# Performance work log

Measured on AMD Instinct MI355X. Metric: run time of the kernel, lower is better.

## Reference

```python
import jax, jax.numpy as jnp
import numpy as np
import math

B, T, C, H = 4, 2048, 1024, 16

def setup_inputs() -> dict:
    key = jax.random.key(0)
    ks = jax.random.split(key, 7)
    s = 0.02
    return {
        'x':  jax.random.normal(ks[0], (B, T, C), dtype=jnp.float32),
        'Wq': jax.random.normal(ks[1], (C, C), dtype=jnp.float32) * s,
        'bq': jnp.zeros((C,), dtype=jnp.float32),
        'Wk': jax.random.normal(ks[2], (C, C), dtype=jnp.float32) * s,
        'bk': jnp.zeros((C,), dtype=jnp.float32),
        'Wv': jax.random.normal(ks[3], (C, C), dtype=jnp.float32) * s,
        'bv': jnp.zeros((C,), dtype=jnp.float32),
    }

def reference(x, Wq, bq, Wk, bk, Wv, bv):
    # Dropouts are identity (eval mode). Note: the original module reuses
    # v_proj as the output projection -- reproduced faithfully.
    b, t, c = x.shape
    hs = c // H
    q = (x @ Wq + bq).reshape(b, t, H, hs).transpose(0, 2, 1, 3)  # [B,H,T,hs]
    k = (x @ Wk + bk).reshape(b, t, H, hs).transpose(0, 2, 1, 3)
    v = (x @ Wv + bv).reshape(b, t, H, hs).transpose(0, 2, 1, 3)
    att = jnp.einsum('bhqd,bhkd->bhqk', q, k) * (1.0 / math.sqrt(hs))
    causal = jnp.tril(jnp.ones((t, t), dtype=bool))
    att = jnp.where(causal[None, None], att, -jnp.inf)
    att = jax.nn.softmax(att, axis=-1)
    y = jnp.einsum('bhqk,bhkd->bhqd', att, v)  # [B,H,T,hs]
    y = y.transpose(0, 2, 1, 3).reshape(b, t, c)
    y = y @ Wv + bv  # module applies v_proj again as output projection
    return y
```

## Files before the change

kernel.cpp:

```cpp
#include <hip/hip_runtime.h>
#include <hip/hip_bf16.h>

typedef __bf16 bf16;
typedef __attribute__((ext_vector_type(8))) __bf16 bf16x8;
typedef __attribute__((ext_vector_type(4))) __bf16 bf16x4;
typedef __attribute__((ext_vector_type(2))) __bf16 bf16x2;
typedef __attribute__((ext_vector_type(4))) float f32x4;
typedef __attribute__((ext_vector_type(2))) unsigned int u32x2;
typedef __attribute__((ext_vector_type(4))) unsigned int u32x4;

#define MFMA16(a, b, c) __builtin_amdgcn_mfma_f32_16x16x32_bf16((a), (b), (c), 0, 0, 0)
#define SM_SCALE 0.18033688011112043f

__device__ __forceinline__ void gld_lds16(const bf16* g, bf16* l) {
    __builtin_amdgcn_global_load_lds((const __attribute__((address_space(1))) void*)g,
                                     (__attribute__((address_space(3))) void*)l, 16, 0, 0);
}

#define PBAR() asm volatile("s_barrier" ::: "memory")
#define VWAIT0() asm volatile("s_waitcnt vmcnt(0)" ::: "memory")

__global__ __launch_bounds__(256) void cvt_x(const float* __restrict__ in,
                                             bf16* __restrict__ outb, int n) {
    int i = (blockIdx.x * 256 + threadIdx.x) * 4;
    if (i + 3 < n) {
        const float4 v = *(const float4*)(in + i);
        bf16x4 o = {(bf16)v.x, (bf16)v.y, (bf16)v.z, (bf16)v.w};
        *(bf16x4*)(outb + i) = o;
    }
}

__global__ __launch_bounds__(256) void transpose_w3(const float* __restrict__ W0,
                                                    const float* __restrict__ W1,
                                                    const float* __restrict__ W2,
                                                    bf16* __restrict__ Wt) {
    const float* W = (blockIdx.z == 0) ? W0 : ((blockIdx.z == 1) ? W1 : W2);
    bf16* dst = Wt + (size_t)blockIdx.z * 1024 * 1024;
    __shared__ float tile[64][65];
    const int r0 = blockIdx.y * 64;
    const int c0 = blockIdx.x * 64;
    const int tid = threadIdx.x;
    for (int i = tid; i < 4096; i += 256) {
        int r = i >> 6, cc = i & 63;
        tile[r][cc] = W[(size_t)(r0 + r) * 1024 + c0 + cc];
    }
    __syncthreads();
    for (int i = tid; i < 4096; i += 256) {
        int n = i >> 6, k = i & 63;
        dst[(size_t)(c0 + n) * 1024 + r0 + k] = (bf16)tile[k][n];
    }
}

__global__ __launch_bounds__(512, 4) void gemm_qkv(const bf16* __restrict__ A,
                                                   const bf16* __restrict__ Bt,
                                                   const float* __restrict__ b0,
                                                   const float* __restrict__ b1,
                                                   const float* __restrict__ b2,
                                                   bf16* __restrict__ qb,
                                                   bf16* __restrict__ kb,
                                                   bf16* __restrict__ Vt) {
    __shared__ alignas(16) bf16 LDS[2 * 12288];

    const int orig = blockIdx.x;
    const int swz = (orig & 7) * 96 + (orig >> 3);
    const int by = swz / 24, bx = swz % 24;
    const int m0 = by * 256, n0 = bx * 128;

    const int tid = threadIdx.x;
    const int wid = tid >> 6, lane = tid & 63;
    const int wr = wid >> 1, wc = wid & 1;
    const int quad = lane >> 4, l16 = lane & 15;

    const int sr = tid >> 2;
    const int scol = (((tid & 3) ^ (sr & 3)) * 8);
    const bf16* gA = A + (size_t)(m0 + sr) * 1024 + scol;
    const bf16* gB = Bt + (size_t)(n0 + sr) * 1024 + scol;
    bf16* lA = &LDS[tid * 8];
    bf16* lB = &LDS[8192 + tid * 8];

    const int coff = ((quad ^ (l16 & 3)) * 8);

    f32x4 acc[4][4] = {};

    auto STAGE = [&](int kt, int p) {
        const int base = p * 12288;
        gld_lds16(gA + kt * 32, lA + base);
        gld_lds16(gA + kt * 32 + (size_t)128 * 1024, lA + base + 4096);
        gld_lds16(gB + kt * 32, lB + base);
    };

    STAGE(0, 0);
    VWAIT0();
    PBAR();

#pragma unroll 1
    for (int kt = 0; kt < 32; kt++) {
        const int p = kt & 1;
        const bf16* Asp = &LDS[p * 12288];
        const bf16* Bsp = Asp + 8192;
        if (kt + 1 < 32) STAGE(kt + 1, p ^ 1);

        bf16x8 af[4], bfr[4];
#pragma unroll
        for (int m4 = 0; m4 < 4; m4++)
            af[m4] = *(const bf16x8*)&Asp[(wr * 64 + m4 * 16 + l16) * 32 + coff];
#pragma unroll
        for (int ni = 0; ni < 4; ni++)
            bfr[ni] = *(const bf16x8*)&Bsp[(wc * 64 + ni * 16 + l16) * 32 + coff];

        __builtin_amdgcn_s_setprio(1);
#pragma unroll
        for (int m4 = 0; m4 < 4; m4++)
#pragma unroll
            for (int ni = 0; ni < 4; ni++)
                acc[m4][ni] = MFMA16(af[m4], bfr[ni], acc[m4][ni]);
        __builtin_amdgcn_s_setprio(0);

        if (kt + 1 < 32) VWAIT0();
        PBAR();
    }

    const int sel = n0 >> 10;
    const int nl0 = (n0 & 1023) + wc * 64;
    const int mb0 = m0 + wr * 64;
    if (sel < 2) {
        const float* bias = (sel == 0) ? b0 : b1;
        bf16* Cp = (sel == 0) ? qb : kb;
        const float qs = (sel == 0) ? SM_SCALE : 1.0f;
#pragma unroll
        for (int mi = 0; mi < 4; mi++) {
            const int mbase = mb0 + mi * 16 + quad * 4;
#pragma unroll
            for (int ni = 0; ni < 4; ni++) {
                const int nl = nl0 + ni * 16 + l16;
                const float bv = bias[nl];
#pragma unroll
                for (int r = 0; r < 4; r++)
                    Cp[(size_t)(mbase + r) * 1024 + nl] = (bf16)((acc[mi][ni][r] + bv) * qs);
            }
        }
    } else {
        const int b = m0 >> 11;
#pragma unroll
        for (int ni = 0; ni < 4; ni++) {
            const int nl = nl0 + ni * 16 + l16;
            const int h = nl >> 6, d = nl & 63;
            const float bv = b2[nl];
            bf16* dst = Vt + ((size_t)(b * 16 + h) * 64 + d) * 2048;
#pragma unroll
            for (int mi = 0; mi < 4; mi++) {
                const int t0 = (mb0 + mi * 16 + quad * 4) & 2047;
                bf16x4 w = {(bf16)(acc[mi][ni][0] + bv), (bf16)(acc[mi][ni][1] + bv),
                            (bf16)(acc[mi][ni][2] + bv), (bf16)(acc[mi][ni][3] + bv)};
                *(bf16x4*)&dst[t0] = w;
            }
        }
    }
}

template <int MODE>
__global__ __launch_bounds__(256) void gemm_bt(const bf16* __restrict__ A,
                                               const bf16* __restrict__ Bt,
                                               const float* __restrict__ b0,
                                               void* __restrict__ out0,
                                               int M, int N, int K) {
    __shared__ alignas(16) bf16 As[128 * 32];
    __shared__ alignas(16) bf16 Bs[128 * 32];
    const int tid = threadIdx.x;
    const int wave = tid >> 6, lane = tid & 63;
    const int quad = lane >> 4, l16 = lane & 15;
    const int m0 = blockIdx.y * 128, n0 = blockIdx.x * 128;
    const int wm = (wave & 1) * 64, wn = (wave >> 1) * 64;

    f32x4 acc[4][4] = {};

    const int srow = lane >> 2, scol = (lane & 3) * 8;
    const bf16* ga = A + (size_t)(m0 + wave * 32 + srow) * K + scol;
    const bf16* gb = Bt + (size_t)(n0 + wave * 32 + srow) * K + scol;
    bf16* la = &As[(wave * 32) * 32];
    bf16* lb = &Bs[(wave * 32) * 32];

    for (int k0 = 0; k0 < K; k0 += 32) {
        __syncthreads();
        gld_lds16(ga + k0, la);
        gld_lds16(ga + k0 + (size_t)16 * K, la + 16 * 32);
        gld_lds16(gb + k0, lb);
        gld_lds16(gb + k0 + (size_t)16 * K, lb + 16 * 32);
        __syncthreads();
        bf16x8 af[4], bfr[4];
#pragma unroll
        for (int mi = 0; mi < 4; mi++)
            af[mi] = *(const bf16x8*)&As[(wm + mi * 16 + l16) * 32 + quad * 8];
#pragma unroll
        for (int ni = 0; ni < 4; ni++)
            bfr[ni] = *(const bf16x8*)&Bs[(wn + ni * 16 + l16) * 32 + quad * 8];
#pragma unroll
        for (int mi = 0; mi < 4; mi++)
#pragma unroll
            for (int ni = 0; ni < 4; ni++)
                acc[mi][ni] = MFMA16(af[mi], bfr[ni], acc[mi][ni]);
    }

    float* Cp = (float*)out0;
#pragma unroll
    for (int mi = 0; mi < 4; mi++) {
        const int mbase = m0 + wm + mi * 16 + quad * 4;
#pragma unroll
        for (int ni = 0; ni < 4; ni++) {
            const int n = n0 + wn + ni * 16 + l16;
            const float bv = b0[n];
#pragma unroll
            for (int r = 0; r < 4; r++)
                Cp[(size_t)(mbase + r) * 1024 + n] = acc[mi][ni][r] + bv;
        }
    }
}

template <bool NEEDMASK>
__device__ __forceinline__ void softmax_reg(const f32x4* st, bf16x8* pf, int qrel) {
    unsigned int p[4][2];
#pragma unroll
    for (int j = 0; j < 4; j++) {
        float pv[4];
#pragma unroll
        for (int r = 0; r < 4; r++) {
            float s = st[j][r];
            if (NEEDMASK && (j * 16 + r > qrel)) s = -1e30f;
            pv[r] = exp2f(s);
        }
        bf16x2 w0 = {(bf16)pv[0], (bf16)pv[1]};
        bf16x2 w1 = {(bf16)pv[2], (bf16)pv[3]};
        p[j][0] = __builtin_bit_cast(unsigned int, w0);
        p[j][1] = __builtin_bit_cast(unsigned int, w1);
    }
#pragma unroll
    for (int ks = 0; ks < 2; ks++) {
        unsigned int q4[4];
#pragma unroll
        for (int h = 0; h < 2; h++) {
            u32x2 s32 = __builtin_amdgcn_permlane32_swap(p[2 * ks][h], p[2 * ks + 1][h],
                                                         false, false);
            u32x2 s16 = __builtin_amdgcn_permlane16_swap(s32[0], s32[1], false, false);
            q4[h] = s16[0];
            q4[2 + h] = s16[1];
        }
        u32x4 qq = {q4[0], q4[1], q4[2], q4[3]};
        pf[ks] = __builtin_bit_cast(bf16x8, qq);
    }
}

__global__ __launch_bounds__(256, 4) void attn(const bf16* __restrict__ Q,
                                               const bf16* __restrict__ Kg,
                                               const bf16* __restrict__ Vt,
                                               bf16* __restrict__ O) {
    const int lin = blockIdx.y * 16 + blockIdx.x;
    const int bh = (lin & 7) * 8 + ((lin >> 3) & 7);
    const int jb = lin >> 6;
    const int b = bh >> 4, h = bh & 15;
    const int tid = threadIdx.x;
    const int wave = tid >> 6, lane = tid & 63;
    const int quad = lane >> 4, l16 = lane & 15;

    __shared__ alignas(16) bf16 KVs[2 * 8192];

    const bf16* Kbase = Kg + ((size_t)b * 2048) * 1024 + h * 64;
    const bf16* Vbase = Vt + (size_t)bh * 64 * 2048;

    const int srow = tid >> 3;
    const int schunk = (tid & 7) ^ (srow & 7);

    const int xorE = (l16 & 7) * 8;
    const int cofA = (quad * 8) ^ xorE;
    const int cofB = (32 + quad * 8) ^ xorE;

    const bf16 one1 = (bf16)1.0f;
    const bf16x8 onesf = {one1, one1, one1, one1, one1, one1, one1, one1};

#pragma unroll 1
    for (int phase = 0; phase < 2; phase++) {
        const int qs = (phase == 0) ? (31 - jb) : jb;
        const int q0 = qs * 64;
        const bf16* Qbase = Q + ((size_t)(b * 2048 + q0)) * 1024 + h * 64;

        bf16x8 qf[2];
#pragma unroll
        for (int ks = 0; ks < 2; ks++)
            qf[ks] = *(const bf16x8*)&Qbase[(size_t)(wave * 16 + l16) * 1024 + ks * 32 + quad * 8];

        f32x4 ot[4] = {};
        f32x4 lacc = {0.f, 0.f, 0.f, 0.f};
        const int ntiles = qs + 1;
        const int qrel = wave * 16 + l16 - quad * 4;

        const bf16* pK = Kbase + (size_t)srow * 1024 + schunk * 8;
        const bf16* pK2 = pK + (size_t)32 * 1024;
        const bf16* pV = Vbase + (size_t)srow * 2048 + schunk * 8;
        const bf16* pV2 = pV + (size_t)32 * 2048;

        {
            bf16* nb = &KVs[tid * 8];
            gld_lds16(pK, nb);
            gld_lds16(pK2, nb + 2048);
            gld_lds16(pV, nb + 4096);
            gld_lds16(pV2, nb + 6144);
            pK += 64 * 1024; pK2 += 64 * 1024; pV += 64; pV2 += 64;
        }
        VWAIT0();
        PBAR();

#pragma unroll 1
        for (int tk = 0; tk < ntiles; tk++) {
            const bf16* buf = &KVs[(tk & 1) * 8192];
            if (tk + 1 < ntiles) {
                bf16* nb = &KVs[((tk + 1) & 1) * 8192 + tid * 8];
                gld_lds16(pK, nb);
                gld_lds16(pK2, nb + 2048);
                gld_lds16(pV, nb + 4096);
                gld_lds16(pV2, nb + 6144);
                pK += 64 * 1024; pK2 += 64 * 1024; pV += 64; pV2 += 64;
            }

            f32x4 st[4] = {};
#pragma unroll
            for (int ks = 0; ks < 2; ks++)
#pragma unroll
                for (int j = 0; j < 4; j++) {
                    const bf16x8 kf =
                        *(const bf16x8*)&buf[(j * 16 + l16) * 64 + (ks ? cofB : cofA)];
                    st[j] = MFMA16(kf, qf[ks], st[j]);
                }

            bf16x8 pf[2];
            if (tk == ntiles - 1)
                softmax_reg<true>(st, pf, qrel);
            else
                softmax_reg<false>(st, pf, qrel);

            lacc = MFMA16(onesf, pf[0], lacc);
            lacc = MFMA16(onesf, pf[1], lacc);

#pragma unroll
            for (int ks = 0; ks < 2; ks++)
#pragma unroll
                for (int db = 0; db < 4; db++) {
                    const bf16x8 vf = *(const bf16x8*)&buf[4096 + (db * 16 + l16) * 64 +
                                                           (ks ? cofB : cofA)];
                    ot[db] = MFMA16(vf, pf[ks], ot[db]);
                }

            if (tk + 1 < ntiles) VWAIT0();
            PBAR();
        }

        const float inv = 1.f / lacc[0];
        bf16* ep = &KVs[(ntiles & 1) * 8192 + wave * (16 * 72)];
#pragma unroll
        for (int db = 0; db < 4; db++) {
            bf16x4 w = {(bf16)(ot[db][0] * inv), (bf16)(ot[db][1] * inv),
                        (bf16)(ot[db][2] * inv), (bf16)(ot[db][3] * inv)};
            *(bf16x4*)&ep[l16 * 72 + db * 16 + quad * 4] = w;
        }
        {
            const int orow = lane >> 2, oc = (lane & 3) * 16;
            bf16* Obase =
                O + ((size_t)(b * 2048 + q0 + wave * 16 + orow)) * 1024 + h * 64 + oc;
            const bf16* src = &ep[orow * 72 + oc];
            *(bf16x8*)&Obase[0] = *(const bf16x8*)&src[0];
            *(bf16x8*)&Obase[8] = *(const bf16x8*)&src[8];
        }
        __syncthreads();
    }
}

extern "C" void kernel_launch(void* const* d_in, const int* in_sizes, int n_in,
                              void* d_out, int out_size, void* d_ws, size_t ws_size,
                              hipStream_t stream) {
    const float* x = (const float*)d_in[0];
    const float* Wq = (const float*)d_in[1];
    const float* bq = (const float*)d_in[2];
    const float* Wk = (const float*)d_in[3];
    const float* bk = (const float*)d_in[4];
    const float* Wv = (const float*)d_in[5];
    const float* bv = (const float*)d_in[6];
    float* out = (float*)d_out;

    const int M = 8192;
    const size_t sz_x = (size_t)M * 1024;
    const size_t sz_w = (size_t)1024 * 1024;

    char* p = (char*)d_ws;
    bf16* xb = (bf16*)p;   p += sz_x * 2;
    bf16* Wcat = (bf16*)p; p += 3 * sz_w * 2;
    bf16* qb = (bf16*)p;   p += sz_x * 2;
    bf16* kb = (bf16*)p;   p += sz_x * 2;
    bf16* Vt = (bf16*)p;   p += sz_x * 2;
    bf16* yatt = (bf16*)p; p += sz_x * 2;

    cvt_x<<<dim3(8192), dim3(256), 0, stream>>>(x, xb, (int)sz_x);
    transpose_w3<<<dim3(16, 16, 3), dim3(256), 0, stream>>>(Wq, Wk, Wv, Wcat);

    gemm_qkv<<<dim3(768), dim3(512), 0, stream>>>(xb, Wcat, bq, bk, bv, qb, kb, Vt);
    attn<<<dim3(16, 64), dim3(256), 0, stream>>>(qb, kb, Vt, yatt);
    gemm_bt<1><<<dim3(8, 64), dim3(256), 0, stream>>>(yatt, Wcat + 2 * sz_w, bv,
                                                      out, M, 1024, 1024);
}
```

Measured before the change: 256.1 us.

## Merge prep kernels, triple-buffer the GEMM, reuse it for output projection

After: 243.5 us. 4.9% less time.

```diff
diff --git a/kernel.cpp b/kernel.cpp
--- a/kernel.cpp
+++ b/kernel.cpp
@@ -19,51 +19,61 @@
 
 #define PBAR() asm volatile("s_barrier" ::: "memory")
 #define VWAIT0() asm volatile("s_waitcnt vmcnt(0)" ::: "memory")
-
-__global__ __launch_bounds__(256) void cvt_x(const float* __restrict__ in,
-                                             bf16* __restrict__ outb, int n) {
-    int i = (blockIdx.x * 256 + threadIdx.x) * 4;
-    if (i + 3 < n) {
-        const float4 v = *(const float4*)(in + i);
-        bf16x4 o = {(bf16)v.x, (bf16)v.y, (bf16)v.z, (bf16)v.w};
-        *(bf16x4*)(outb + i) = o;
-    }
-}
-
-__global__ __launch_bounds__(256) void transpose_w3(const float* __restrict__ W0,
-                                                    const float* __restrict__ W1,
-                                                    const float* __restrict__ W2,
-                                                    bf16* __restrict__ Wt) {
-    const float* W = (blockIdx.z == 0) ? W0 : ((blockIdx.z == 1) ? W1 : W2);
-    bf16* dst = Wt + (size_t)blockIdx.z * 1024 * 1024;
+#define VWAIT3() asm volatile("s_waitcnt vmcnt(3)" ::: "memory")
+
+__global__ __launch_bounds__(256) void prep(const float* __restrict__ W0,
+                                            const float* __restrict__ W1,
+                                            const float* __restrict__ W2,
+                                            bf16* __restrict__ Wt,
+                                            const float* __restrict__ xin,
+                                            bf16* __restrict__ xout) {
     __shared__ float tile[64][65];
-    const int r0 = blockIdx.y * 64;
-    const int c0 = blockIdx.x * 64;
+    const int blk = blockIdx.x;
     const int tid = threadIdx.x;
-    for (int i = tid; i < 4096; i += 256) {
-        int r = i >> 6, cc = i & 63;
-        tile[r][cc] = W[(size_t)(r0 + r) * 1024 + c0 + cc];
-    }
-    __syncthreads();
-    for (int i = tid; i < 4096; i += 256) {
-        int n = i >> 6, k = i & 63;
-        dst[(size_t)(c0 + n) * 1024 + r0 + k] = (bf16)tile[k][n];
-    }
-}
-
-__global__ __launch_bounds__(512, 4) void gemm_qkv(const bf16* __restrict__ A,
-                                                   const bf16* __restrict__ Bt,
-                                                   const float* __restrict__ b0,
-                                                   const float* __restrict__ b1,
-                                                   const float* __restrict__ b2,
-                                                   bf16* __restrict__ qb,
-                                                   bf16* __restrict__ kb,
-                                                   bf16* __restrict__ Vt) {
-    __shared__ alignas(16) bf16 LDS[2 * 12288];
+    if (blk < 768) {
+        const int z = blk >> 8, rem = blk & 255;
+        const int r0 = (rem >> 4) * 64;
+        const int c0 = (rem & 15) * 64;
+        const float* W = (z == 0) ? W0 : ((z == 1) ? W1 : W2);
+        bf16* dst = Wt + (size_t)z * 1024 * 1024;
+        for (int i = tid; i < 4096; i += 256) {
+            int r = i >> 6, cc = i & 63;
+            tile[r][cc] = W[(size_t)(r0 + r) * 1024 + c0 + cc];
+        }
+        __syncthreads();
+        for (int i = tid; i < 4096; i += 256) {
+            int n = i >> 6, k = i & 63;
+            dst[(size_t)(c0 + n) * 1024 + r0 + k] = (bf16)tile[k][n];
+        }
+    } else {
+        const size_t i0 = ((size_t)(blk - 768) * 256 + tid) * 16;
+#pragma unroll
+        for (int j = 0; j < 2; j++) {
+            const float4 v0 = *(const float4*)(xin + i0 + j * 8);
+            const float4 v1 = *(const float4*)(xin + i0 + j * 8 + 4);
+            bf16x8 o = {(bf16)v0.x, (bf16)v0.y, (bf16)v0.z, (bf16)v0.w,
+                        (bf16)v1.x, (bf16)v1.y, (bf16)v1.z, (bf16)v1.w};
+            *(bf16x8*)(xout + i0 + j * 8) = o;
+        }
+    }
+}
+
+template <int MODE>
+__global__ __launch_bounds__(512, 4) void gemm_main(const bf16* __restrict__ A,
+                                                    const bf16* __restrict__ Bt,
+                                                    const float* __restrict__ b0,
+                                                    const float* __restrict__ b1,
+                                                    const float* __restrict__ b2,
+                                                    void* __restrict__ out0,
+                                                    void* __restrict__ out1,
+                                                    void* __restrict__ out2,
+                                                    int nbx) {
+    __shared__ alignas(16) bf16 LDS[3 * 12288];
 
     const int orig = blockIdx.x;
-    const int swz = (orig & 7) * 96 + (orig >> 3);
-    const int by = swz / 24, bx = swz % 24;
+    const int chunk = (int)gridDim.x >> 3;
+    const int swz = (orig & 7) * chunk + (orig >> 3);
+    const int by = swz / nbx, bx = swz % nbx;
     const int m0 = by * 256, n0 = bx * 128;
 
     const int tid = threadIdx.x;
@@ -90,15 +100,17 @@
     };
 
     STAGE(0, 0);
-    VWAIT0();
+    STAGE(1, 1);
+    VWAIT3();
     PBAR();
 
+    int rb = 0;
+    int sb = 2;
 #pragma unroll 1
     for (int kt = 0; kt < 32; kt++) {
-        const int p = kt & 1;
-        const bf16* Asp = &LDS[p * 12288];
+        const bf16* Asp = &LDS[rb * 12288];
         const bf16* Bsp = Asp + 8192;
-        if (kt + 1 < 32) STAGE(kt + 1, p ^ 1);
+        if (kt + 2 < 32) STAGE(kt + 2, sb);
 
         bf16x8 af[4], bfr[4];
 #pragma unroll
@@ -116,102 +128,69 @@
                 acc[m4][ni] = MFMA16(af[m4], bfr[ni], acc[m4][ni]);
         __builtin_amdgcn_s_setprio(0);
 
-        if (kt + 1 < 32) VWAIT0();
-        PBAR();
-    }
-
-    const int sel = n0 >> 10;
+        if (kt < 30) {
+            VWAIT3();
+            PBAR();
+        } else if (kt == 30) {
+            VWAIT0();
+            PBAR();
+        }
+        rb = (rb == 2) ? 0 : rb + 1;
+        sb = (sb == 2) ? 0 : sb + 1;
+    }
+
     const int nl0 = (n0 & 1023) + wc * 64;
     const int mb0 = m0 + wr * 64;
-    if (sel < 2) {
-        const float* bias = (sel == 0) ? b0 : b1;
-        bf16* Cp = (sel == 0) ? qb : kb;
-        const float qs = (sel == 0) ? SM_SCALE : 1.0f;
+    if (MODE == 0) {
+        const int sel = n0 >> 10;
+        if (sel < 2) {
+            const float* bias = (sel == 0) ? b0 : b1;
+            bf16* Cp = (bf16*)((sel == 0) ? out0 : out1);
+            const float qs = (sel == 0) ? SM_SCALE : 1.0f;
+#pragma unroll
+            for (int mi = 0; mi < 4; mi++) {
+                const int mbase = mb0 + mi * 16 + quad * 4;
+#pragma unroll
+                for (int ni = 0; ni < 4; ni++) {
+                    const int nl = nl0 + ni * 16 + l16;
+                    const float bv = bias[nl];
+#pragma unroll
+                    for (int r = 0; r < 4; r++)
+                        Cp[(size_t)(mbase + r) * 1024 + nl] =
+                            (bf16)((acc[mi][ni][r] + bv) * qs);
+                }
+            }
+        } else {
+            bf16* Vt = (bf16*)out2;
+            const int b = m0 >> 11;
+#pragma unroll
+            for (int ni = 0; ni < 4; ni++) {
+                const int nl = nl0 + ni * 16 + l16;
+                const int h = nl >> 6, d = nl & 63;
+                const float bv = b2[nl];
+                bf16* dst = Vt + ((size_t)(b * 16 + h) * 64 + d) * 2048;
+#pragma unroll
+                for (int mi = 0; mi < 4; mi++) {
+                    const int t0 = (mb0 + mi * 16 + quad * 4) & 2047;
+                    bf16x4 w = {(bf16)(acc[mi][ni][0] + bv), (bf16)(acc[mi][ni][1] + bv),
+                                (bf16)(acc[mi][ni][2] + bv), (bf16)(acc[mi][ni][3] + bv)};
+                    *(bf16x4*)&dst[t0] = w;
+                }
+            }
+        }
+    } else {
+        float* Cp = (float*)out0;
 #pragma unroll
         for (int mi = 0; mi < 4; mi++) {
             const int mbase = mb0 + mi * 16 + quad * 4;
 #pragma unroll
             for (int ni = 0; ni < 4; ni++) {
-                const int nl = nl0 + ni * 16 + l16;
-                const float bv = bias[nl];
+                const int n = n0 + wc * 64 + ni * 16 + l16;
+                const float bv = b0[n];
 #pragma unroll
                 for (int r = 0; r < 4; r++)
-                    Cp[(size_t)(mbase + r) * 1024 + nl] = (bf16)((acc[mi][ni][r] + bv) * qs);
+                    Cp[(size_t)(mbase + r) * 1024 + n] = acc[mi][ni][r] + bv;
             }
-        }
-    } else {
-        const int b = m0 >> 11;
-#pragma unroll
-        for (int ni = 0; ni < 4; ni++) {
-            const int nl = nl0 + ni * 16 + l16;
-            const int h = nl >> 6, d = nl & 63;
-            const float bv = b2[nl];
-            bf16* dst = Vt + ((size_t)(b * 16 + h) * 64 + d) * 2048;
-#pragma unroll
-            for (int mi = 0; mi < 4; mi++) {
-                const int t0 = (mb0 + mi * 16 + quad * 4) & 2047;
-                bf16x4 w = {(bf16)(acc[mi][ni][0] + bv), (bf16)(acc[mi][ni][1] + bv),
-                            (bf16)(acc[mi][ni][2] + bv), (bf16)(acc[mi][ni][3] + bv)};
-                *(bf16x4*)&dst[t0] = w;
-            }
-        }
-    }
-}
-
-template <int MODE>
-__global__ __launch_bounds__(256) void gemm_bt(const bf16* __restrict__ A,
-                                               const bf16* __restrict__ Bt,
-                                               const float* __restrict__ b0,
-                                               void* __restrict__ out0,
-                                               int M, int N, int K) {
-    __shared__ alignas(16) bf16 As[128 * 32];
-    __shared__ alignas(16) bf16 Bs[128 * 32];
-    const int tid = threadIdx.x;
-    const int wave = tid >> 6, lane = tid & 63;
-    const int quad = lane >> 4, l16 = lane & 15;
-    const int m0 = blockIdx.y * 128, n0 = blockIdx.x * 128;
-    const int wm = (wave & 1) * 64, wn = (wave >> 1) * 64;
-
-    f32x4 acc[4][4] = {};
-
-    const int srow = lane >> 2, scol = (lane & 3) * 8;
-    const bf16* ga = A + (size_t)(m0 + wave * 32 + srow) * K + scol;
-    const bf16* gb = Bt + (size_t)(n0 + wave * 32 + srow) * K + scol;
-    bf16* la = &As[(wave * 32) * 32];
-    bf16* lb = &Bs[(wave * 32) * 32];
-
-    for (int k0 = 0; k0 < K; k0 += 32) {
-        __syncthreads();
-        gld_lds16(ga + k0, la);
-        gld_lds16(ga + k0 + (size_t)16 * K, la + 16 * 32);
-        gld_lds16(gb + k0, lb);
-        gld_lds16(gb + k0 + (size_t)16 * K, lb + 16 * 32);
-        __syncthreads();
-        bf16x8 af[4], bfr[4];
-#pragma unroll
-        for (int mi = 0; mi < 4; mi++)
-            af[mi] = *(const bf16x8*)&As[(wm + mi * 16 + l16) * 32 + quad * 8];
-#pragma unroll
-        for (int ni = 0; ni < 4; ni++)
-            bfr[ni] = *(const bf16x8*)&Bs[(wn + ni * 16 + l16) * 32 + quad * 8];
-#pragma unroll
-        for (int mi = 0; mi < 4; mi++)
-#pragma unroll
-            for (int ni = 0; ni < 4; ni++)
-                acc[mi][ni] = MFMA16(af[mi], bfr[ni], acc[mi][ni]);
-    }
-
-    float* Cp = (float*)out0;
-#pragma unroll
-    for (int mi = 0; mi < 4; mi++) {
-        const int mbase = m0 + wm + mi * 16 + quad * 4;
-#pragma unroll
-        for (int ni = 0; ni < 4; ni++) {
-            const int n = n0 + wn + ni * 16 + l16;
-            const float bv = b0[n];
-#pragma unroll
-            for (int r = 0; r < 4; r++)
-                Cp[(size_t)(mbase + r) * 1024 + n] = acc[mi][ni][r] + bv;
         }
     }
 }
@@ -396,11 +375,10 @@
     bf16* Vt = (bf16*)p;   p += sz_x * 2;
     bf16* yatt = (bf16*)p; p += sz_x * 2;
 
-    cvt_x<<<dim3(8192), dim3(256), 0, stream>>>(x, xb, (int)sz_x);
-    transpose_w3<<<dim3(16, 16, 3), dim3(256), 0, stream>>>(Wq, Wk, Wv, Wcat);
-
-    gemm_qkv<<<dim3(768), dim3(512), 0, stream>>>(xb, Wcat, bq, bk, bv, qb, kb, Vt);
+    prep<<<dim3(2816), dim3(256), 0, stream>>>(Wq, Wk, Wv, Wcat, x, xb);
+
+    gemm_main<0><<<dim3(768), dim3(512), 0, stream>>>(xb, Wcat, bq, bk, bv, qb, kb, Vt, 24);
     attn<<<dim3(16, 64), dim3(256), 0, stream>>>(qb, kb, Vt, yatt);
-    gemm_bt<1><<<dim3(8, 64), dim3(256), 0, stream>>>(yatt, Wcat + 2 * sz_w, bv,
-                                                      out, M, 1024, 1024);
-}
+    gemm_main<1><<<dim3(256), dim3(512), 0, stream>>>(yatt, Wcat + 2 * sz_w, bv, bv, bv,
+                                                      out, out, out, 8);
+}
```
